# Kernel tuning notes

Hardware: AMD Instinct MI355X
Metric: run time of the kernel (lower is better)

The kernel has to match this reference:

```python
import jax, jax.numpy as jnp
import numpy as np

N_NODES = 50000
N_EDGES = 800000
IN_CH = 128
HID = 64
HEADS = 4
OUT_CH = 1
NEG_SLOPE = 0.2  # PyG GATConv default


def setup_inputs() -> dict:
    key = jax.random.key(0)
    ks = jax.random.split(key, 16)
    s = 0.1
    x = jax.random.normal(ks[0], (N_NODES, IN_CH), dtype=jnp.float32)
    edge_index = jax.random.randint(ks[1], (2, N_EDGES), 0, N_NODES, dtype=jnp.int64)
    # GATConv 1: in=128 -> 64 per head, 4 heads, concat
    W1 = jax.random.normal(ks[2], (IN_CH, HEADS * HID), dtype=jnp.float32) * s
    att_src1 = jax.random.normal(ks[3], (HEADS, HID), dtype=jnp.float32) * s
    att_dst1 = jax.random.normal(ks[4], (HEADS, HID), dtype=jnp.float32) * s
    b1 = jnp.zeros((HEADS * HID,), dtype=jnp.float32)
    # GATConv 2: in=256 -> 64, 1 head, mean (concat=False)
    W2 = jax.random.normal(ks[5], (HEADS * HID, HID), dtype=jnp.float32) * s
    att_src2 = jax.random.normal(ks[6], (1, HID), dtype=jnp.float32) * s
    att_dst2 = jax.random.normal(ks[7], (1, HID), dtype=jnp.float32) * s
    b2 = jnp.zeros((HID,), dtype=jnp.float32)
    # MLP: Linear(128,64) -> ReLU -> Linear(64,1)
    mlp_w1 = jax.random.normal(ks[8], (2 * HID, HID), dtype=jnp.float32) * s
    mlp_b1 = jnp.zeros((HID,), dtype=jnp.float32)
    mlp_w2 = jax.random.normal(ks[9], (HID, OUT_CH), dtype=jnp.float32) * s
    mlp_b2 = jnp.zeros((OUT_CH,), dtype=jnp.float32)
    return dict(x=x, edge_index=edge_index, W1=W1, att_src1=att_src1,
                att_dst1=att_dst1, b1=b1, W2=W2, att_src2=att_src2,
                att_dst2=att_dst2, b2=b2, mlp_w1=mlp_w1, mlp_b1=mlp_b1,
                mlp_w2=mlp_w2, mlp_b2=mlp_b2)


def gat_layer(x, edge_index, W, att_src, att_dst, bias, heads, ch, concat):
    N = x.shape[0]
    # add self loops (PyG default add_self_loops=True)
    loop = jnp.arange(N, dtype=edge_index.dtype)
    src = jnp.concatenate([edge_index[0], loop])
    dst = jnp.concatenate([edge_index[1], loop])
    h = (x @ W).reshape(N, heads, ch)                      # [N,H,C]
    a_src = jnp.einsum('nhc,hc->nh', h, att_src)           # [N,H]
    a_dst = jnp.einsum('nhc,hc->nh', h, att_dst)
    logits = jax.nn.leaky_relu(a_src[src] + a_dst[dst], NEG_SLOPE)  # [E,H]
    # segment softmax over destination node
    m = jax.ops.segment_max(logits, dst, num_segments=N)
    e = jnp.exp(logits - m[dst])
    denom = jax.ops.segment_sum(e, dst, num_segments=N)
    alpha = e / denom[dst]                                 # [E,H]
    msg = alpha[:, :, None] * h[src]                       # [E,H,C]
    out = jax.ops.segment_sum(msg, dst, num_segments=N)    # [N,H,C]
    out = out.reshape(N, heads * ch) if concat else out.mean(axis=1)
    return out + bias


def reference(x, edge_index, W1, att_src1, att_dst1, b1,
              W2, att_src2, att_dst2, b2,
              mlp_w1, mlp_b1, mlp_w2, mlp_b2):
    # eval mode: dropouts are identity
    h = gat_layer(x, edge_index, W1, att_src1, att_dst1, b1, HEADS, HID, True)
    h = jax.nn.elu(h)
    h = gat_layer(h, edge_index, W2, att_src2, att_dst2, b2, 1, HID, False)
    u = h[edge_index[0]]                                   # [E,HID]
    v = h[edge_index[1]]
    ef = jnp.concatenate([u, v], axis=1)                   # [E,2*HID]
    hid = jax.nn.relu(ef @ mlp_w1 + mlp_b1)
    return hid @ mlp_w2 + mlp_b2                           # [E,OUT_CH]
```

## Files before the change

### kernel.cpp

```cpp
#include <hip/hip_runtime.h>
#include <hip/hip_bf16.h>
#include <math.h>

#define NN 50000
#define NE 800000
#define NB ((NN + 255) / 256)
#define NEG 0.2f

typedef __hip_bfloat16 bf16;
typedef __attribute__((ext_vector_type(8))) short s8v;
typedef __attribute__((ext_vector_type(4))) float f4v;

__device__ __forceinline__ float bf2f(unsigned short u) {
  union { unsigned int i; float f; } c;
  c.i = ((unsigned int)u) << 16;
  return c.f;
}
__device__ __forceinline__ float blo(unsigned int u) {
  union { unsigned int i; float f; } c;
  c.i = u << 16;
  return c.f;
}
__device__ __forceinline__ float bhi(unsigned int u) {
  union { unsigned int i; float f; } c;
  c.i = u & 0xffff0000u;
  return c.f;
}
__device__ __forceinline__ unsigned short f2b(float f) {
  bf16 b = __float2bfloat16(f);
  return __builtin_bit_cast(unsigned short, b);
}
__device__ __forceinline__ float lrelu(float t) { return (t > 0.f) ? t : NEG * t; }

__global__ void zero_counts_k(int* __restrict__ c) {
  int i = blockIdx.x * 256 + threadIdx.x;
  if (i < NN) c[i] = 0;
}

__global__ void hist_k(const int* __restrict__ ei, int* __restrict__ counts) {
  int e = blockIdx.x * 256 + threadIdx.x;
  if (e >= NE) return;
  atomicAdd(&counts[ei[NE + e]], 1);
}

__global__ __launch_bounds__(256) void scan_bsum_k(const int* __restrict__ counts,
                                                   int* __restrict__ bsums) {
  __shared__ int wsum[4];
  int i = blockIdx.x * 256 + threadIdx.x;
  int v = (i < NN) ? counts[i] : 0;
#pragma unroll
  for (int off = 32; off; off >>= 1) v += __shfl_xor(v, off);
  if ((threadIdx.x & 63) == 0) wsum[threadIdx.x >> 6] = v;
  __syncthreads();
  if (threadIdx.x == 0) bsums[blockIdx.x] = wsum[0] + wsum[1] + wsum[2] + wsum[3];
}

__global__ __launch_bounds__(256) void scan_top_k(int* __restrict__ bsums) {
  __shared__ int s[256];
  int t = threadIdx.x;
  int v = (t < NB) ? bsums[t] : 0;
  s[t] = v;
  __syncthreads();
  for (int off = 1; off < 256; off <<= 1) {
    int u = (t >= off) ? s[t - off] : 0;
    __syncthreads();
    s[t] += u;
    __syncthreads();
  }
  if (t < NB) bsums[t] = s[t] - v;
}

__global__ __launch_bounds__(256) void scan_final_k(const int* __restrict__ counts,
                                                    const int* __restrict__ bsums,
                                                    int* __restrict__ offsets,
                                                    int* __restrict__ cursor) {
  __shared__ int s[256];
  int t = threadIdx.x;
  int i = blockIdx.x * 256 + t;
  int v = (i < NN) ? counts[i] : 0;
  s[t] = v;
  __syncthreads();
  for (int off = 1; off < 256; off <<= 1) {
    int u = (t >= off) ? s[t - off] : 0;
    __syncthreads();
    s[t] += u;
    __syncthreads();
  }
  int excl = s[t] - v + bsums[blockIdx.x];
  if (i < NN) {
    offsets[i] = excl;
    cursor[i] = excl;
    if (i == NN - 1) offsets[NN] = excl + v;
  }
}

__global__ void scatter_k(const int* __restrict__ ei, int* __restrict__ cursor,
                          int2* __restrict__ csr) {
  int e = blockIdx.x * 256 + threadIdx.x;
  if (e >= NE) return;
  int s = ei[e], d = ei[NE + e];
  int pos = atomicAdd(&cursor[d], 1);
  csr[pos] = make_int2(s, e);
}

__global__ void convx_k(const float* __restrict__ in, unsigned short* __restrict__ out,
                        int n4) {
  int i = blockIdx.x * 256 + threadIdx.x;
  if (i >= n4) return;
  float4 v = *(const float4*)(in + (size_t)i * 4);
  ushort4 o = {f2b(v.x), f2b(v.y), f2b(v.z), f2b(v.w)};
  *(ushort4*)(out + (size_t)i * 4) = o;
}

__global__ void convT_k(const float* __restrict__ in, unsigned short* __restrict__ out,
                        int K, int N) {
  int i = blockIdx.x * 256 + threadIdx.x;
  if (i >= K * N) return;
  int n = i / K, k = i - n * K;
  out[i] = f2b(in[(size_t)k * N + n]);
}

__global__ void convPQ_k(const float* __restrict__ mw1, unsigned short* __restrict__ out) {
  int i = blockIdx.x * 256 + threadIdx.x;
  if (i >= 128 * 64) return;
  int n = i >> 6, k = i & 63;
  float v = (n < 64) ? mw1[(size_t)k * 64 + n] : mw1[(size_t)(64 + k) * 64 + (n - 64)];
  out[i] = f2b(v);
}

template <int DOTS>
__global__ __launch_bounds__(256) void mgemm_k(
    const unsigned short* __restrict__ A, int lda,
    const unsigned short* __restrict__ Bt, int ldb,
    unsigned short* __restrict__ C, int ldc,
    int M, int N, int K,
    const float* __restrict__ ws, const float* __restrict__ wd,
    float* __restrict__ as_, float* __restrict__ ad_, int H) {
  __shared__ unsigned short Asl[64][40];
  __shared__ unsigned short Btl[64][40];
  __shared__ float sdot[64], ddot[64];
  int bm = blockIdx.y * 64, bn = blockIdx.x * 64;
  int t = threadIdx.x;
  int wv = t >> 6, lane = t & 63;
  int wm = (wv >> 1) * 32, wn = (wv & 1) * 32;
  int l16 = lane & 15, lq = lane >> 4;
  if (DOTS && t < 64) { sdot[t] = 0.f; ddot[t] = 0.f; }
  f4v acc[2][2];
#pragma unroll
  for (int mi = 0; mi < 2; ++mi)
#pragma unroll
    for (int ni = 0; ni < 2; ++ni) {
      acc[mi][ni][0] = 0.f; acc[mi][ni][1] = 0.f;
      acc[mi][ni][2] = 0.f; acc[mi][ni][3] = 0.f;
    }
  int sr = t >> 2, sc = (t & 3) * 8;
  for (int k0 = 0; k0 < K; k0 += 32) {
    uint4 av = {0, 0, 0, 0};
    int gr = bm + sr;
    if (gr < M) av = *(const uint4*)(A + (size_t)gr * lda + k0 + sc);
    *(uint4*)&Asl[sr][sc] = av;
    uint4 bv = *(const uint4*)(Bt + (size_t)(bn + sr) * ldb + k0 + sc);
    *(uint4*)&Btl[sr][sc] = bv;
    __syncthreads();
    s8v af[2], bfv[2];
#pragma unroll
    for (int mi = 0; mi < 2; ++mi)
      af[mi] = *(const s8v*)&Asl[wm + mi * 16 + l16][lq * 8];
#pragma unroll
    for (int ni = 0; ni < 2; ++ni)
      bfv[ni] = *(const s8v*)&Btl[wn + ni * 16 + l16][lq * 8];
#pragma unroll
    for (int mi = 0; mi < 2; ++mi)
#pragma unroll
      for (int ni = 0; ni < 2; ++ni)
        acc[mi][ni] = __builtin_amdgcn_mfma_f32_16x16x32_bf16(
            af[mi], bfv[ni], acc[mi][ni], 0, 0, 0);
    __syncthreads();
  }
#pragma unroll
  for (int mi = 0; mi < 2; ++mi)
#pragma unroll
    for (int rr = 0; rr < 4; ++rr) {
      int row = bm + wm + mi * 16 + lq * 4 + rr;
      if (row < M) {
#pragma unroll
        for (int ni = 0; ni < 2; ++ni) {
          int col = bn + wn + ni * 16 + l16;
          C[(size_t)row * ldc + col] = f2b(acc[mi][ni][rr]);
        }
      }
    }
  if (DOTS) {
    int head = blockIdx.x;
    float ps[2][4], pd[2][4];
#pragma unroll
    for (int mi = 0; mi < 2; ++mi)
#pragma unroll
      for (int rr = 0; rr < 4; ++rr) {
        float s = 0.f, d = 0.f;
#pragma unroll
        for (int ni = 0; ni < 2; ++ni) {
          int col = wn + ni * 16 + l16;
          s += acc[mi][ni][rr] * ws[head * 64 + col];
          d += acc[mi][ni][rr] * wd[head * 64 + col];
        }
        ps[mi][rr] = s;
        pd[mi][rr] = d;
      }
#pragma unroll
    for (int off = 1; off < 16; off <<= 1)
#pragma unroll
      for (int mi = 0; mi < 2; ++mi)
#pragma unroll
        for (int rr = 0; rr < 4; ++rr) {
          ps[mi][rr] += __shfl_xor(ps[mi][rr], off);
          pd[mi][rr] += __shfl_xor(pd[mi][rr], off);
        }
    if (l16 == 0) {
#pragma unroll
      for (int mi = 0; mi < 2; ++mi)
#pragma unroll
        for (int rr = 0; rr < 4; ++rr) {
          int rl = wm + mi * 16 + lq * 4 + rr;
          atomicAdd(&sdot[rl], ps[mi][rr]);
          atomicAdd(&ddot[rl], pd[mi][rr]);
        }
    }
    __syncthreads();
    if (t < 64 && bm + t < M) {
      as_[(size_t)(bm + t) * H + head] = sdot[t];
      ad_[(size_t)(bm + t) * H + head] = ddot[t];
    }
  }
}

__global__ __launch_bounds__(256) void gat_agg4_k(
    const int* __restrict__ offsets, const int2* __restrict__ csr,
    const unsigned short* __restrict__ h, const float* __restrict__ as_,
    const float* __restrict__ ad_, const float* __restrict__ bias,
    unsigned short* __restrict__ out) {
  __shared__ float exs[4][64][4];
  __shared__ int srcs[4][64];
  int wvx = threadIdx.x >> 6, lane = threadIdx.x & 63;
  int n = blockIdx.x * 4 + wvx;
  int hd = lane >> 4;
  int beg = offsets[n], end = offsets[n + 1];
  float4 adn = *(const float4*)(ad_ + (size_t)n * 4);
  float4 asn = *(const float4*)(as_ + (size_t)n * 4);
  float es0 = __expf(lrelu(asn.x + adn.x));
  float es1 = __expf(lrelu(asn.y + adn.y));
  float es2 = __expf(lrelu(asn.z + adn.z));
  float es3 = __expf(lrelu(asn.w + adn.w));
  float d0 = es0, d1 = es1, d2 = es2, d3 = es3;
  float wself = (hd == 0) ? es0 : (hd == 1) ? es1 : (hd == 2) ? es2 : es3;
  uint2 sv = *(const uint2*)(h + (size_t)n * 256 + lane * 4);
  float2 a01, a23;
  a01.x = wself * blo(sv.x); a01.y = wself * bhi(sv.x);
  a23.x = wself * blo(sv.y); a23.y = wself * bhi(sv.y);
  for (int base = beg; base < end; base += 64) {
    int cnt = min(64, end - base);
    int src = 0;
    float e0 = 0.f, e1 = 0.f, e2 = 0.f, e3 = 0.f;
    if (lane < cnt) {
      src = csr[base + lane].x;
      float4 a4 = *(const float4*)(as_ + (size_t)src * 4);
      e0 = __expf(lrelu(a4.x + adn.x));
      e1 = __expf(lrelu(a4.y + adn.y));
      e2 = __expf(lrelu(a4.z + adn.z));
      e3 = __expf(lrelu(a4.w + adn.w));
    }
    float s0 = e0, s1 = e1, s2 = e2, s3 = e3;
#pragma unroll
    for (int off = 32; off; off >>= 1) {
      s0 += __shfl_xor(s0, off);
      s1 += __shfl_xor(s1, off);
      s2 += __shfl_xor(s2, off);
      s3 += __shfl_xor(s3, off);
    }
    d0 += s0; d1 += s1; d2 += s2; d3 += s3;
    float4 ex4 = {e0, e1, e2, e3};
    *(float4*)(&exs[wvx][lane][0]) = ex4;
    srcs[wvx][lane] = src;
    __builtin_amdgcn_wave_barrier();
    int e = 0;
    for (; e + 8 <= cnt; e += 8) {
      uint2 r[8];
      float w[8];
#pragma unroll
      for (int j = 0; j < 8; ++j) {
        int si = srcs[wvx][e + j];
        w[j] = exs[wvx][e + j][hd];
        r[j] = *(const uint2*)(h + (size_t)si * 256 + lane * 4);
      }
#pragma unroll
      for (int j = 0; j < 8; ++j) {
        a01.x += w[j] * blo(r[j].x); a01.y += w[j] * bhi(r[j].x);
        a23.x += w[j] * blo(r[j].y); a23.y += w[j] * bhi(r[j].y);
      }
    }
    for (; e < cnt; ++e) {
      int si = srcs[wvx][e];
      float w = exs[wvx][e][hd];
      uint2 r = *(const uint2*)(h + (size_t)si * 256 + lane * 4);
      a01.x += w * blo(r.x); a01.y += w * bhi(r.x);
      a23.x += w * blo(r.y); a23.y += w * bhi(r.y);
    }
  }
  float myden = (hd == 0) ? d0 : (hd == 1) ? d1 : (hd == 2) ? d2 : d3;
  float inv = 1.f / myden;
  float4 b4 = *(const float4*)(bias + lane * 4);
  float4 res;
  res.x = a01.x * inv + b4.x;
  res.y = a01.y * inv + b4.y;
  res.z = a23.x * inv + b4.z;
  res.w = a23.y * inv + b4.w;
  res.x = (res.x > 0.f) ? res.x : (__expf(res.x) - 1.f);
  res.y = (res.y > 0.f) ? res.y : (__expf(res.y) - 1.f);
  res.z = (res.z > 0.f) ? res.z : (__expf(res.z) - 1.f);
  res.w = (res.w > 0.f) ? res.w : (__expf(res.w) - 1.f);
  ushort4 ov = {f2b(res.x), f2b(res.y), f2b(res.z), f2b(res.w)};
  *(ushort4*)(out + (size_t)n * 256 + lane * 4) = ov;
}

__global__ __launch_bounds__(256) void gat_agg1_k(
    const int* __restrict__ offsets, const int2* __restrict__ csr,
    const unsigned short* __restrict__ h, const float* __restrict__ as_,
    const float* __restrict__ ad_, const float* __restrict__ bias,
    unsigned short* __restrict__ out) {
  __shared__ float exs[4][64];
  __shared__ int srcs[4][64];
  int wvx = threadIdx.x >> 6, lane = threadIdx.x & 63;
  int n = blockIdx.x * 4 + wvx;
  int slot = lane >> 5, cp = lane & 31;
  int beg = offsets[n], end = offsets[n + 1];
  float adn = ad_[n];
  float eself = __expf(lrelu(as_[n] + adn));
  float den = eself;
  float ax = 0.f, ay = 0.f;
  if (slot == 0) {
    unsigned int sv = *(const unsigned int*)(h + (size_t)n * 64 + cp * 2);
    ax = eself * blo(sv);
    ay = eself * bhi(sv);
  }
  for (int base = beg; base < end; base += 64) {
    int cnt = min(64, end - base);
    int src = 0;
    float ex = 0.f;
    if (lane < cnt) {
      src = csr[base + lane].x;
      ex = __expf(lrelu(as_[src] + adn));
    }
    float s = ex;
#pragma unroll
    for (int off = 32; off; off >>= 1) s += __shfl_xor(s, off);
    den += s;
    exs[wvx][lane] = ex;
    srcs[wvx][lane] = src;
    __builtin_amdgcn_wave_barrier();
    int e = 0;
    for (; e + 8 <= cnt; e += 8) {
      int i0 = e + slot, i1 = e + 2 + slot, i2 = e + 4 + slot, i3 = e + 6 + slot;
      int si0 = srcs[wvx][i0], si1 = srcs[wvx][i1], si2 = srcs[wvx][i2], si3 = srcs[wvx][i3];
      float w0 = exs[wvx][i0], w1 = exs[wvx][i1], w2 = exs[wvx][i2], w3 = exs[wvx][i3];
      unsigned int r0 = *(const unsigned int*)(h + (size_t)si0 * 64 + cp * 2);
      unsigned int r1 = *(const unsigned int*)(h + (size_t)si1 * 64 + cp * 2);
      unsigned int r2 = *(const unsigned int*)(h + (size_t)si2 * 64 + cp * 2);
      unsigned int r3 = *(const unsigned int*)(h + (size_t)si3 * 64 + cp * 2);
      ax += w0 * blo(r0); ay += w0 * bhi(r0);
      ax += w1 * blo(r1); ay += w1 * bhi(r1);
      ax += w2 * blo(r2); ay += w2 * bhi(r2);
      ax += w3 * blo(r3); ay += w3 * bhi(r3);
    }
    for (; e < cnt; e += 2) {
      int i = e + slot;
      int ok = (i < cnt);
      int si = srcs[wvx][ok ? i : 0];
      float w = ok ? exs[wvx][i] : 0.f;
      unsigned int r = *(const unsigned int*)(h + (size_t)si * 64 + cp * 2);
      ax += w * blo(r); ay += w * bhi(r);
    }
  }
  ax += __shfl_xor(ax, 32);
  ay += __shfl_xor(ay, 32);
  if (slot == 0) {
    float inv = 1.f / den;
    ushort2 ov;
    ov.x = f2b(ax * inv + bias[cp * 2]);
    ov.y = f2b(ay * inv + bias[cp * 2 + 1]);
    *(ushort2*)(out + (size_t)n * 64 + cp * 2) = ov;
  }
}

__global__ __launch_bounds__(256) void edge_out_k(
    const int* __restrict__ offsets, const int2* __restrict__ csr,
    const unsigned short* __restrict__ pq,
    const float* __restrict__ mb1, const float* __restrict__ w2,
    const float* __restrict__ mb2, float* __restrict__ out) {
  int wvx = threadIdx.x >> 6, lane = threadIdx.x & 63;
  int n = blockIdx.x * 4 + wvx;
  int slot = lane >> 4, cp = lane & 15;
  int beg = offsets[n], end = offsets[n + 1];
  ushort4 qv = *(const ushort4*)(pq + (size_t)n * 128 + 64 + cp * 4);
  float4 base4 = *(const float4*)(mb1 + cp * 4);
  base4.x += bf2f(qv.x); base4.y += bf2f(qv.y);
  base4.z += bf2f(qv.z); base4.w += bf2f(qv.w);
  float4 w4 = *(const float4*)(w2 + cp * 4);
  float b2v = mb2[0];
  for (int base = beg; base < end; base += 4) {
    int i = base + slot;
    int2 se = {0, 0};
    bool ok = (i < end);
    if (ok) se = csr[i];
    float r = 0.f;
    if (ok) {
      ushort4 pv = *(const ushort4*)(pq + (size_t)se.x * 128 + cp * 4);
      float v0 = fmaxf(bf2f(pv.x) + base4.x, 0.f);
      float v1 = fmaxf(bf2f(pv.y) + base4.y, 0.f);
      float v2 = fmaxf(bf2f(pv.z) + base4.z, 0.f);
      float v3 = fmaxf(bf2f(pv.w) + base4.w, 0.f);
      r = v0 * w4.x + v1 * w4.y + v2 * w4.z + v3 * w4.w;
    }
    r += __shfl_xor(r, 8);
    r += __shfl_xor(r, 4);
    r += __shfl_xor(r, 2);
    r += __shfl_xor(r, 1);
    if (cp == 0 && ok) out[se.y] = r + b2v;
  }
}

extern "C" void kernel_launch(void* const* d_in, const int* in_sizes, int n_in,
                              void* d_out, int out_size, void* d_ws, size_t ws_size,
                              hipStream_t stream) {
  const float* x = (const float*)d_in[0];
  const int* ei = (const int*)d_in[1];
  const float* W1 = (const float*)d_in[2];
  const float* as1w = (const float*)d_in[3];
  const float* ad1w = (const float*)d_in[4];
  const float* b1 = (const float*)d_in[5];
  const float* W2 = (const float*)d_in[6];
  const float* as2w = (const float*)d_in[7];
  const float* ad2w = (const float*)d_in[8];
  const float* b2 = (const float*)d_in[9];
  const float* mw1 = (const float*)d_in[10];
  const float* mb1 = (const float*)d_in[11];
  const float* mw2 = (const float*)d_in[12];
  const float* mb2 = (const float*)d_in[13];
  float* out = (float*)d_out;

  char* ws = (char*)d_ws;
  size_t o = 0;
  auto alloc = [&](size_t bytes) {
    void* ptr = ws + o;
    o += (bytes + 255) & ~(size_t)255;
    return ptr;
  };
  int* counts = (int*)alloc((size_t)NN * 4);
  int* offsets = (int*)alloc((size_t)(NN + 1) * 4);
  int* cursor = (int*)alloc((size_t)NN * 4);
  int* bsums = (int*)alloc((size_t)NB * 4);
  int2* csr = (int2*)alloc((size_t)NE * 8);
  unsigned short* xb = (unsigned short*)alloc((size_t)NN * 128 * 2);
  unsigned short* w1t = (unsigned short*)alloc((size_t)256 * 128 * 2);
  unsigned short* w2t = (unsigned short*)alloc((size_t)64 * 256 * 2);
  unsigned short* pqt = (unsigned short*)alloc((size_t)128 * 64 * 2);
  unsigned short* h1b = (unsigned short*)alloc((size_t)NN * 256 * 2);
  float* a_s1 = (float*)alloc((size_t)NN * 4 * 4);
  float* a_d1 = (float*)alloc((size_t)NN * 4 * 4);
  unsigned short* x2b = (unsigned short*)alloc((size_t)NN * 256 * 2);
  unsigned short* yb = (unsigned short*)alloc((size_t)NN * 64 * 2);
  unsigned short* h2b = h1b;
  unsigned short* pq = h1b + (size_t)NN * 64;

  zero_counts_k<<<NB, 256, 0, stream>>>(counts);
  hist_k<<<(NE + 255) / 256, 256, 0, stream>>>(ei, counts);
  scan_bsum_k<<<NB, 256, 0, stream>>>(counts, bsums);
  scan_top_k<<<1, 256, 0, stream>>>(bsums);
  scan_final_k<<<NB, 256, 0, stream>>>(counts, bsums, offsets, cursor);
  scatter_k<<<(NE + 255) / 256, 256, 0, stream>>>(ei, cursor, csr);

  convx_k<<<(NN * 32 + 255) / 256, 256, 0, stream>>>(x, xb, NN * 32);
  convT_k<<<(256 * 128 + 255) / 256, 256, 0, stream>>>(W1, w1t, 128, 256);
  convT_k<<<(64 * 256 + 255) / 256, 256, 0, stream>>>(W2, w2t, 256, 64);
  convPQ_k<<<(128 * 64 + 255) / 256, 256, 0, stream>>>(mw1, pqt);

  int gy = (NN + 63) / 64;
  mgemm_k<1><<<dim3(4, gy), 256, 0, stream>>>(xb, 128, w1t, 128, h1b, 256,
                                              NN, 256, 128, as1w, ad1w, a_s1, a_d1, 4);
  gat_agg4_k<<<NN / 4, 256, 0, stream>>>(offsets, csr, h1b, a_s1, a_d1, b1, x2b);

  mgemm_k<1><<<dim3(1, gy), 256, 0, stream>>>(x2b, 256, w2t, 256, h2b, 64,
                                              NN, 64, 256, as2w, ad2w, a_s1, a_d1, 1);
  gat_agg1_k<<<NN / 4, 256, 0, stream>>>(offsets, csr, h2b, a_s1, a_d1, b2, yb);

  mgemm_k<0><<<dim3(2, gy), 256, 0, stream>>>(yb, 64, pqt, 64, pq, 128,
                                              NN, 128, 64, nullptr, nullptr,
                                              nullptr, nullptr, 0);

  edge_out_k<<<NN / 4, 256, 0, stream>>>(offsets, csr, pq, mb1, mw2, mb2, out);
}
```

Measured before the change: 295.3 us.

## Fuse conversion kernels, fold top-level scan, and retune aggregation loops

```diff
diff --git a/kernel.cpp b/kernel.cpp
--- a/kernel.cpp
+++ b/kernel.cpp
@@ -31,11 +31,6 @@
   return __builtin_bit_cast(unsigned short, b);
 }
 __device__ __forceinline__ float lrelu(float t) { return (t > 0.f) ? t : NEG * t; }
-
-__global__ void zero_counts_k(int* __restrict__ c) {
-  int i = blockIdx.x * 256 + threadIdx.x;
-  if (i < NN) c[i] = 0;
-}
 
 __global__ void hist_k(const int* __restrict__ ei, int* __restrict__ counts) {
   int e = blockIdx.x * 256 + threadIdx.x;
@@ -55,27 +50,20 @@
   if (threadIdx.x == 0) bsums[blockIdx.x] = wsum[0] + wsum[1] + wsum[2] + wsum[3];
 }
 
-__global__ __launch_bounds__(256) void scan_top_k(int* __restrict__ bsums) {
-  __shared__ int s[256];
-  int t = threadIdx.x;
-  int v = (t < NB) ? bsums[t] : 0;
-  s[t] = v;
-  __syncthreads();
-  for (int off = 1; off < 256; off <<= 1) {
-    int u = (t >= off) ? s[t - off] : 0;
-    __syncthreads();
-    s[t] += u;
-    __syncthreads();
-  }
-  if (t < NB) bsums[t] = s[t] - v;
-}
-
 __global__ __launch_bounds__(256) void scan_final_k(const int* __restrict__ counts,
                                                     const int* __restrict__ bsums,
                                                     int* __restrict__ offsets,
                                                     int* __restrict__ cursor) {
   __shared__ int s[256];
+  __shared__ int wsum[4];
+  __shared__ int bpref;
   int t = threadIdx.x;
+  int bv = (t < NB && t < (int)blockIdx.x) ? bsums[t] : 0;
+#pragma unroll
+  for (int off = 32; off; off >>= 1) bv += __shfl_xor(bv, off);
+  if ((t & 63) == 0) wsum[t >> 6] = bv;
+  __syncthreads();
+  if (t == 0) bpref = wsum[0] + wsum[1] + wsum[2] + wsum[3];
   int i = blockIdx.x * 256 + t;
   int v = (i < NN) ? counts[i] : 0;
   s[t] = v;
@@ -86,7 +74,7 @@
     s[t] += u;
     __syncthreads();
   }
-  int excl = s[t] - v + bsums[blockIdx.x];
+  int excl = s[t] - v + bpref;
   if (i < NN) {
     offsets[i] = excl;
     cursor[i] = excl;
@@ -103,29 +91,39 @@
   csr[pos] = make_int2(s, e);
 }
 
-__global__ void convx_k(const float* __restrict__ in, unsigned short* __restrict__ out,
-                        int n4) {
+#define NX4 (NN * 32)
+#define NW1 (256 * 128)
+#define NW2 (64 * 256)
+#define NPQ (128 * 64)
+__global__ void conv_all_k(const float* __restrict__ x, const float* __restrict__ W1,
+                           const float* __restrict__ W2, const float* __restrict__ mw1,
+                           unsigned short* __restrict__ xb, unsigned short* __restrict__ w1t,
+                           unsigned short* __restrict__ w2t, unsigned short* __restrict__ pqt) {
   int i = blockIdx.x * 256 + threadIdx.x;
-  if (i >= n4) return;
-  float4 v = *(const float4*)(in + (size_t)i * 4);
-  ushort4 o = {f2b(v.x), f2b(v.y), f2b(v.z), f2b(v.w)};
-  *(ushort4*)(out + (size_t)i * 4) = o;
-}
-
-__global__ void convT_k(const float* __restrict__ in, unsigned short* __restrict__ out,
-                        int K, int N) {
-  int i = blockIdx.x * 256 + threadIdx.x;
-  if (i >= K * N) return;
-  int n = i / K, k = i - n * K;
-  out[i] = f2b(in[(size_t)k * N + n]);
-}
-
-__global__ void convPQ_k(const float* __restrict__ mw1, unsigned short* __restrict__ out) {
-  int i = blockIdx.x * 256 + threadIdx.x;
-  if (i >= 128 * 64) return;
-  int n = i >> 6, k = i & 63;
-  float v = (n < 64) ? mw1[(size_t)k * 64 + n] : mw1[(size_t)(64 + k) * 64 + (n - 64)];
-  out[i] = f2b(v);
+  if (i < NX4) {
+    float4 v = *(const float4*)(x + (size_t)i * 4);
+    ushort4 o = {f2b(v.x), f2b(v.y), f2b(v.z), f2b(v.w)};
+    *(ushort4*)(xb + (size_t)i * 4) = o;
+    return;
+  }
+  i -= NX4;
+  if (i < NW1) {
+    int n = i >> 7, k = i & 127;
+    w1t[i] = f2b(W1[(size_t)k * 256 + n]);
+    return;
+  }
+  i -= NW1;
+  if (i < NW2) {
+    int n = i >> 8, k = i & 255;
+    w2t[i] = f2b(W2[(size_t)k * 64 + n]);
+    return;
+  }
+  i -= NW2;
+  if (i < NPQ) {
+    int n = i >> 6, k = i & 63;
+    float v = (n < 64) ? mw1[(size_t)k * 64 + n] : mw1[(size_t)(64 + k) * 64 + (n - 64)];
+    pqt[i] = f2b(v);
+  }
 }
 
 template <int DOTS>
@@ -283,19 +281,28 @@
     srcs[wvx][lane] = src;
     __builtin_amdgcn_wave_barrier();
     int e = 0;
-    for (; e + 8 <= cnt; e += 8) {
-      uint2 r[8];
-      float w[8];
-#pragma unroll
-      for (int j = 0; j < 8; ++j) {
-        int si = srcs[wvx][e + j];
-        w[j] = exs[wvx][e + j][hd];
-        r[j] = *(const uint2*)(h + (size_t)si * 256 + lane * 4);
+    for (; e + 16 <= cnt; e += 16) {
+      uint2 r[16];
+#pragma unroll
+      for (int j = 0; j < 16; ++j)
+        r[j] = *(const uint2*)(h + (size_t)srcs[wvx][e + j] * 256 + lane * 4);
+#pragma unroll
+      for (int j = 0; j < 16; ++j) {
+        float w = exs[wvx][e + j][hd];
+        a01.x += w * blo(r[j].x); a01.y += w * bhi(r[j].x);
+        a23.x += w * blo(r[j].y); a23.y += w * bhi(r[j].y);
       }
-#pragma unroll
-      for (int j = 0; j < 8; ++j) {
-        a01.x += w[j] * blo(r[j].x); a01.y += w[j] * bhi(r[j].x);
-        a23.x += w[j] * blo(r[j].y); a23.y += w[j] * bhi(r[j].y);
+    }
+    for (; e + 4 <= cnt; e += 4) {
+      uint2 r[4];
+#pragma unroll
+      for (int j = 0; j < 4; ++j)
+        r[j] = *(const uint2*)(h + (size_t)srcs[wvx][e + j] * 256 + lane * 4);
+#pragma unroll
+      for (int j = 0; j < 4; ++j) {
+        float w = exs[wvx][e + j][hd];
+        a01.x += w * blo(r[j].x); a01.y += w * bhi(r[j].x);
+        a23.x += w * blo(r[j].y); a23.y += w * bhi(r[j].y);
       }
     }
     for (; e < cnt; ++e) {
@@ -331,16 +338,16 @@
   __shared__ int srcs[4][64];
   int wvx = threadIdx.x >> 6, lane = threadIdx.x & 63;
   int n = blockIdx.x * 4 + wvx;
-  int slot = lane >> 5, cp = lane & 31;
+  int slot = lane >> 4, cp = lane & 15;
   int beg = offsets[n], end = offsets[n + 1];
   float adn = ad_[n];
   float eself = __expf(lrelu(as_[n] + adn));
   float den = eself;
-  float ax = 0.f, ay = 0.f;
+  float2 a01 = {0.f, 0.f}, a23 = {0.f, 0.f};
   if (slot == 0) {
-    unsigned int sv = *(const unsigned int*)(h + (size_t)n * 64 + cp * 2);
-    ax = eself * blo(sv);
-    ay = eself * bhi(sv);
+    uint2 sv = *(const uint2*)(h + (size_t)n * 64 + cp * 4);
+    a01.x = eself * blo(sv.x); a01.y = eself * bhi(sv.x);
+    a23.x = eself * blo(sv.y); a23.y = eself * bhi(sv.y);
   }
   for (int base = beg; base < end; base += 64) {
     int cnt = min(64, end - base);
@@ -357,37 +364,48 @@
     exs[wvx][lane] = ex;
     srcs[wvx][lane] = src;
     __builtin_amdgcn_wave_barrier();
-    int e = 0;
-    for (; e + 8 <= cnt; e += 8) {
-      int i0 = e + slot, i1 = e + 2 + slot, i2 = e + 4 + slot, i3 = e + 6 + slot;
-      int si0 = srcs[wvx][i0], si1 = srcs[wvx][i1], si2 = srcs[wvx][i2], si3 = srcs[wvx][i3];
+    int i = slot;
+    for (; i + 12 < cnt; i += 16) {
+      uint2 r[4];
+      int i0 = i, i1 = i + 4, i2 = i + 8, i3 = i + 12;
+      r[0] = *(const uint2*)(h + (size_t)srcs[wvx][i0] * 64 + cp * 4);
+      r[1] = *(const uint2*)(h + (size_t)srcs[wvx][i1] * 64 + cp * 4);
+      r[2] = *(const uint2*)(h + (size_t)srcs[wvx][i2] * 64 + cp * 4);
+      r[3] = *(const uint2*)(h + (size_t)srcs[wvx][i3] * 64 + cp * 4);
       float w0 = exs[wvx][i0], w1 = exs[wvx][i1], w2 = exs[wvx][i2], w3 = exs[wvx][i3];
-      unsigned int r0 = *(const unsigned int*)(h + (size_t)si0 * 64 + cp * 2);
-      unsigned int r1 = *(const unsigned int*)(h + (size_t)si1 * 64 + cp * 2);
-      unsigned int r2 = *(const unsigned int*)(h + (size_t)si2 * 64 + cp * 2);
-      unsigned int r3 = *(const unsigned int*)(h + (size_t)si3 * 64 + cp * 2);
-      ax += w0 * blo(r0); ay += w0 * bhi(r0);
-      ax += w1 * blo(r1); ay += w1 * bhi(r1);
-      ax += w2 * blo(r2); ay += w2 * bhi(r2);
-      ax += w3 * blo(r3); ay += w3 * bhi(r3);
-    }
-    for (; e < cnt; e += 2) {
-      int i = e + slot;
-      int ok = (i < cnt);
-      int si = srcs[wvx][ok ? i : 0];
-      float w = ok ? exs[wvx][i] : 0.f;
-      unsigned int r = *(const unsigned int*)(h + (size_t)si * 64 + cp * 2);
-      ax += w * blo(r); ay += w * bhi(r);
-    }
-  }
-  ax += __shfl_xor(ax, 32);
-  ay += __shfl_xor(ay, 32);
+      a01.x += w0 * blo(r[0].x); a01.y += w0 * bhi(r[0].x);
+      a23.x += w0 * blo(r[0].y); a23.y += w0 * bhi(r[0].y);
+      a01.x += w1 * blo(r[1].x); a01.y += w1 * bhi(r[1].x);
+      a23.x += w1 * blo(r[1].y); a23.y += w1 * bhi(r[1].y);
+      a01.x += w2 * blo(r[2].x); a01.y += w2 * bhi(r[2].x);
+      a23.x += w2 * blo(r[2].y); a23.y += w2 * bhi(r[2].y);
+      a01.x += w3 * blo(r[3].x); a01.y += w3 * bhi(r[3].x);
+      a23.x += w3 * blo(r[3].y); a23.y += w3 * bhi(r[3].y);
+    }
+    for (; i < cnt; i += 4) {
+      int si = srcs[wvx][i];
+      float w = exs[wvx][i];
+      uint2 r = *(const uint2*)(h + (size_t)si * 64 + cp * 4);
+      a01.x += w * blo(r.x); a01.y += w * bhi(r.x);
+      a23.x += w * blo(r.y); a23.y += w * bhi(r.y);
+    }
+  }
+#pragma unroll
+  for (int off = 16; off <= 32; off <<= 1) {
+    a01.x += __shfl_xor(a01.x, off);
+    a01.y += __shfl_xor(a01.y, off);
+    a23.x += __shfl_xor(a23.x, off);
+    a23.y += __shfl_xor(a23.y, off);
+  }
   if (slot == 0) {
     float inv = 1.f / den;
-    ushort2 ov;
-    ov.x = f2b(ax * inv + bias[cp * 2]);
-    ov.y = f2b(ay * inv + bias[cp * 2 + 1]);
-    *(ushort2*)(out + (size_t)n * 64 + cp * 2) = ov;
+    float4 b4 = *(const float4*)(bias + cp * 4);
+    ushort4 ov;
+    ov.x = f2b(a01.x * inv + b4.x);
+    ov.y = f2b(a01.y * inv + b4.y);
+    ov.z = f2b(a23.x * inv + b4.z);
+    ov.w = f2b(a23.y * inv + b4.w);
+    *(ushort4*)(out + (size_t)n * 64 + cp * 4) = ov;
   }
 }
 
@@ -471,17 +489,14 @@
   unsigned short* h2b = h1b;
   unsigned short* pq = h1b + (size_t)NN * 64;
 
-  zero_counts_k<<<NB, 256, 0, stream>>>(counts);
+  hipMemsetAsync(counts, 0, (size_t)NN * 4, stream);
   hist_k<<<(NE + 255) / 256, 256, 0, stream>>>(ei, counts);
   scan_bsum_k<<<NB, 256, 0, stream>>>(counts, bsums);
-  scan_top_k<<<1, 256, 0, stream>>>(bsums);
   scan_final_k<<<NB, 256, 0, stream>>>(counts, bsums, offsets, cursor);
   scatter_k<<<(NE + 255) / 256, 256, 0, stream>>>(ei, cursor, csr);
 
-  convx_k<<<(NN * 32 + 255) / 256, 256, 0, stream>>>(x, xb, NN * 32);
-  convT_k<<<(256 * 128 + 255) / 256, 256, 0, stream>>>(W1, w1t, 128, 256);
-  convT_k<<<(64 * 256 + 255) / 256, 256, 0, stream>>>(W2, w2t, 256, 64);
-  convPQ_k<<<(128 * 64 + 255) / 256, 256, 0, stream>>>(mw1, pqt);
+  conv_all_k<<<(NX4 + NW1 + NW2 + NPQ + 255) / 256, 256, 0, stream>>>(
+      x, W1, W2, mw1, xb, w1t, w2t, pqt);
 
   int gy = (NN + 63) / 64;
   mgemm_k<1><<<dim3(4, gy), 256, 0, stream>>>(xb, 128, w1t, 128, h1b, 256,
```

Measured after the change: 302.4 us. 1.02x slower.
